# Optimization experiments

Measured on AMD Instinct MI355X. Metric: run time of the kernel, lower is better.

## Reference

```python
import jax, jax.numpy as jnp
import numpy as np
import math

N, D, H, DK, DV, FF = 2048, 1024, 16, 64, 64, 4096
EPS = 1e-5


def setup_inputs() -> dict:
    key = jax.random.key(0)
    ks = jax.random.split(key, 10)
    s = 0.02  # scaled init for numerical stability (original uses torch.randn)
    return {
        "x": jax.random.normal(ks[0], (N, D), dtype=jnp.float32),
        # per-head projections stacked: [H, D, DK/DV]
        "w_q": jax.random.normal(ks[1], (H, D, DK), dtype=jnp.float32) * s,
        "w_k": jax.random.normal(ks[2], (H, D, DK), dtype=jnp.float32) * s,
        "w_v": jax.random.normal(ks[3], (H, D, DV), dtype=jnp.float32) * s,
        "w_o": jax.random.normal(ks[4], (H * DV, D), dtype=jnp.float32) * s,
        "ln1_g": jnp.ones((D,), jnp.float32),
        "ln1_b": jnp.zeros((D,), jnp.float32),
        # FFN: Linear stored as [in, out] so y = x @ w + b
        "w1": jax.random.normal(ks[5], (D, FF), dtype=jnp.float32) * s,
        "b1": jnp.zeros((FF,), jnp.float32),
        "w2": jax.random.normal(ks[6], (FF, D), dtype=jnp.float32) * s,
        "b2": jnp.zeros((D,), jnp.float32),
        "ln2_g": jnp.ones((D,), jnp.float32),
        "ln2_b": jnp.zeros((D,), jnp.float32),
    }


def _layernorm(x, g, b):
    mu = jnp.mean(x, axis=-1, keepdims=True)
    var = jnp.mean(jnp.square(x - mu), axis=-1, keepdims=True)
    return (x - mu) * jax.lax.rsqrt(var + EPS) * g + b


def reference(x, w_q, w_k, w_v, w_o, ln1_g, ln1_b, w1, b1, w2, b2, ln2_g, ln2_b):
    n = x.shape[0]
    # multi-head causal self-attention (heads batched instead of Python loop)
    q = jnp.einsum('nd,hdk->hnk', x, w_q)  # [H,N,DK]
    k = jnp.einsum('nd,hdk->hnk', x, w_k)
    v = jnp.einsum('nd,hdv->hnv', x, w_v)
    scores = jnp.einsum('hnk,hmk->hnm', q, k) / math.sqrt(DK)  # [H,N,N]
    causal = jnp.tril(jnp.ones((n, n), dtype=bool))
    scores = jnp.where(causal, scores, -jnp.inf)
    probs = jax.nn.softmax(scores, axis=-1)
    attn = jnp.einsum('hnm,hmv->hnv', probs, v)  # [H,N,DV]
    concat = jnp.transpose(attn, (1, 0, 2)).reshape(n, H * DV)  # head-order concat
    mha = concat @ w_o  # [N,D]
    # residual + LN, FFN (note: ReLU after BOTH linears, as in the source)
    h = _layernorm(x + mha, ln1_g, ln1_b)
    ff = jax.nn.relu(jax.nn.relu(h @ w1 + b1) @ w2 + b2)
    return _layernorm(h + ff, ln2_g, ln2_b)
```

## Files before the change

kernel.cpp:

```cpp
#include <hip/hip_runtime.h>
#include <math.h>


#define NTOK   2048
#define DMODEL 1024
#define NHEAD  16
#define DHEAD  64
#define DFF    4096
#define LNEPS  1e-5f

typedef unsigned int   u32;
typedef unsigned short u16;
typedef _Float16       f16;
typedef __attribute__((ext_vector_type(8))) short short8;
typedef __attribute__((ext_vector_type(4))) float f32x4;
typedef __attribute__((ext_vector_type(4))) _Float16 f16x4;

__device__ __forceinline__ u16 f2b(float f) {
    u32 b = __float_as_uint(f);
    b += 0x7FFFu + ((b >> 16) & 1u);
    return (u16)(b >> 16);
}
__device__ __forceinline__ float b2f(u16 v) {
    return __uint_as_float((u32)v << 16);
}

#define AS1(p) ((const __attribute__((address_space(1))) u32*)(p))
#define AS3(p) ((__attribute__((address_space(3))) u32*)(p))

template<int RELU, int BIAS, int RESID, int OUT_BF16, int SPLITK>
__global__ __launch_bounds__(256) void mfma_gemm(
    const u16* __restrict__ A, int lda,
    const u16* __restrict__ Bt, int ldbt,
    void* __restrict__ Cp, int ldc, int Kc,
    const float* __restrict__ bias,
    const float* __restrict__ resid, int ldr,
    size_t pstride)
{
    __shared__ u16 As[2][128 * 32];
    __shared__ u16 Bs[2][128 * 32];

    const int tid = threadIdx.x;
    const int l = tid & 63, w = tid >> 6;
    const int row0 = blockIdx.y * 128, col0 = blockIdx.x * 128;
    const int kbase = (SPLITK > 1) ? blockIdx.z * Kc : 0;

    f32x4 acc[4][4];
    #pragma unroll
    for (int m = 0; m < 4; ++m)
        #pragma unroll
        for (int n = 0; n < 4; ++n)
            acc[m][n] = (f32x4){0.f, 0.f, 0.f, 0.f};

    const int srow = w * 32 + (l >> 2);
    const int skk  = (l & 3) * 8;
    const u16* Ag = A  + (size_t)(row0 + srow) * lda  + kbase + skk;
    const u16* Bg = Bt + (size_t)(col0 + srow) * ldbt + kbase + skk;

    const int fr  = l & 15;
    const int fk  = (l >> 4) * 8;
    const int ar0 = (w >> 1) * 64;
    const int bc0 = (w & 1) * 64;

    auto STAGE = [&](int buf, int k0) {
        char* AsB = (char*)&As[buf][0] + w * 2048;
        char* BsB = (char*)&Bs[buf][0] + w * 2048;
        __builtin_amdgcn_global_load_lds(AS1(Ag + k0),                     AS3(AsB),        16, 0, 0);
        __builtin_amdgcn_global_load_lds(AS1(Ag + k0 + (size_t)16 * lda),  AS3(AsB + 1024), 16, 0, 0);
        __builtin_amdgcn_global_load_lds(AS1(Bg + k0),                     AS3(BsB),        16, 0, 0);
        __builtin_amdgcn_global_load_lds(AS1(Bg + k0 + (size_t)16 * ldbt), AS3(BsB + 1024), 16, 0, 0);
    };

    STAGE(0, 0);
    int cur = 0;
    for (int k0 = 0; k0 < Kc; k0 += 32) {
        __syncthreads();
        if (k0 + 32 < Kc) STAGE(cur ^ 1, k0 + 32);

        short8 af[4], bfr[4];
        #pragma unroll
        for (int m = 0; m < 4; ++m)
            af[m] = *reinterpret_cast<const short8*>(&As[cur][(ar0 + m * 16 + fr) * 32 + fk]);
        #pragma unroll
        for (int n = 0; n < 4; ++n)
            bfr[n] = *reinterpret_cast<const short8*>(&Bs[cur][(bc0 + n * 16 + fr) * 32 + fk]);
        #pragma unroll
        for (int m = 0; m < 4; ++m)
            #pragma unroll
            for (int n = 0; n < 4; ++n)
                acc[m][n] = __builtin_amdgcn_mfma_f32_16x16x32_bf16(af[m], bfr[n], acc[m][n], 0, 0, 0);
        cur ^= 1;
    }

    if (SPLITK > 1) {
        f16* Pp = (f16*)Cp + blockIdx.z * pstride;
        #pragma unroll
        for (int m = 0; m < 4; ++m)
            #pragma unroll
            for (int n = 0; n < 4; ++n)
                #pragma unroll
                for (int r = 0; r < 4; ++r) {
                    int row = row0 + ar0 + m * 16 + (l >> 4) * 4 + r;
                    int col = col0 + bc0 + n * 16 + (l & 15);
                    Pp[(size_t)row * ldc + col] = (f16)acc[m][n][r];
                }
        return;
    }

    #pragma unroll
    for (int m = 0; m < 4; ++m) {
        #pragma unroll
        for (int n = 0; n < 4; ++n) {
            #pragma unroll
            for (int r = 0; r < 4; ++r) {
                int row = row0 + ar0 + m * 16 + (l >> 4) * 4 + r;
                int col = col0 + bc0 + n * 16 + (l & 15);
                float val = acc[m][n][r];
                if (BIAS)  val += bias[col];
                if (RESID) val += resid[(size_t)row * ldr + col];
                if (RELU)  val = fmaxf(val, 0.0f);
                if (OUT_BF16) ((u16*)Cp)[(size_t)row * ldc + col] = f2b(val);
                else          ((float*)Cp)[(size_t)row * ldc + col] = val;
            }
        }
    }
}

__device__ __forceinline__ void transpose_tile32(
    const float* __restrict__ in, int ldin,
    u16* __restrict__ out, int ldout, int r0, int c0)
{
    __shared__ float tile[32][33];
    int tx = threadIdx.x & 31, ty = threadIdx.x >> 5;
    #pragma unroll
    for (int i = 0; i < 4; ++i) {
        int r = ty + i * 8;
        tile[r][tx] = in[(size_t)(r0 + r) * ldin + c0 + tx];
    }
    __syncthreads();
    #pragma unroll
    for (int i = 0; i < 4; ++i) {
        int rr = ty + i * 8;
        out[(size_t)(c0 + rr) * ldout + r0 + tx] = f2b(tile[tx][rr]);
    }
}

__global__ __launch_bounds__(256) void prep_all(
    const float* __restrict__ x,
    const float* __restrict__ wq, const float* __restrict__ wk, const float* __restrict__ wv,
    const float* __restrict__ wo, const float* __restrict__ w1, const float* __restrict__ w2,
    u16* __restrict__ xb, u16* __restrict__ wqkvT, u16* __restrict__ woT,
    u16* __restrict__ w1T, u16* __restrict__ w2T)
{
    int b = blockIdx.x;
    if (b < 1024) {
        int i = (b * 256 + threadIdx.x) * 8;
        float4 v0 = *reinterpret_cast<const float4*>(x + i);
        float4 v1 = *reinterpret_cast<const float4*>(x + i + 4);
        ushort4 o0, o1;
        o0.x = f2b(v0.x); o0.y = f2b(v0.y); o0.z = f2b(v0.z); o0.w = f2b(v0.w);
        o1.x = f2b(v1.x); o1.y = f2b(v1.y); o1.z = f2b(v1.z); o1.w = f2b(v1.w);
        *reinterpret_cast<ushort4*>(xb + i)     = o0;
        *reinterpret_cast<ushort4*>(xb + i + 4) = o1;
    } else if (b < 4096) {
        int u = b - 1024;
        int z = u >> 6, t = u & 63;
        int p = z >> 4, hh = z & 15;
        const float* in = (p == 0 ? wq : p == 1 ? wk : wv) + (size_t)hh * DMODEL * DHEAD;
        u16* out = wqkvT + (size_t)(p * 1024 + hh * 64) * DMODEL;
        transpose_tile32(in, DHEAD, out, DMODEL, (t >> 1) * 32, (t & 1) * 32);
    } else if (b < 5120) {
        int u = b - 4096;
        transpose_tile32(wo, DMODEL, woT, DMODEL, (u >> 5) * 32, (u & 31) * 32);
    } else if (b < 9216) {
        int u = b - 5120;
        transpose_tile32(w1, DFF, w1T, DMODEL, (u >> 7) * 32, (u & 127) * 32);
    } else {
        int u = b - 9216;
        transpose_tile32(w2, DMODEL, w2T, DFF, (u >> 5) * 32, (u & 31) * 32);
    }
}

__global__ __launch_bounds__(512) void flash_attn_mfma(
    const u16* __restrict__ qkvb, u16* __restrict__ concatb)
{
    const int bid = blockIdx.x;
    const int lo = bid & 255;
    int it = lo >> 3;
    int h  = lo & 7;
    if (bid >= 256) { it = 31 - it; h += 8; }

    const u16* qh = qkvb + h * DHEAD;
    const u16* kh = qkvb + DMODEL + h * DHEAD;
    const u16* vh = qkvb + 2 * DMODEL + h * DHEAD;
    const int LDQ = 3 * DMODEL;

    const float SC2  = 0.18033688f;
    const float THR2 = 11.541560f;

    __shared__ u16 Ks[4][64][72];
    __shared__ u16 Vt[4][64][72];

    const int tid = threadIdx.x;
    const int l = tid & 63, w = tid >> 6;
    const int grp = w >> 2, wq = w & 3;
    const int fr = l & 15, fg = l >> 4;

    short8 qf[2];
    {
        const u16* qp = qh + (size_t)(it * 64 + wq * 16 + fr) * LDQ + fg * 8;
        qf[0] = *reinterpret_cast<const short8*>(qp);
        qf[1] = *reinterpret_cast<const short8*>(qp + 32);
    }

    const int kr  = tid >> 1;
    const int kb  = kr >> 6, krl = kr & 63;
    const int kc  = (tid & 1) * 32;
    const int vp  = tid >> 2;
    const int vb  = vp >> 5, vpl = vp & 31;
    const int vc  = (tid & 3) * 16;

    short8 kf[4], vf0[2], vf1[2];
    auto PREFETCH = [&](int s) {
        const u16* kg = kh + (size_t)(s * 256 + kr) * LDQ + kc;
        kf[0] = *reinterpret_cast<const short8*>(kg);
        kf[1] = *reinterpret_cast<const short8*>(kg + 8);
        kf[2] = *reinterpret_cast<const short8*>(kg + 16);
        kf[3] = *reinterpret_cast<const short8*>(kg + 24);
        const u16* vg = vh + (size_t)(s * 256 + 2 * vp) * LDQ + vc;
        vf0[0] = *reinterpret_cast<const short8*>(vg);
        vf0[1] = *reinterpret_cast<const short8*>(vg + 8);
        vf1[0] = *reinterpret_cast<const short8*>(vg + LDQ);
        vf1[1] = *reinterpret_cast<const short8*>(vg + LDQ + 8);
    };

    f32x4 o[4];
    #pragma unroll
    for (int n = 0; n < 4; ++n) o[n] = (f32x4){0.f, 0.f, 0.f, 0.f};
    float m_run = -INFINITY, l_run = 0.0f;

    const int sA = fr + 16 * ((2 * fg) & 3);
    const int sB = sA + 16;
    const bool hi = (fg >= 2);

    char* VtSb = (char*)&Vt[vb][0][0];

    const int niter = (it >> 2) + 1;
    PREFETCH(0);

    for (int s = 0; s < niter; ++s) {
        __syncthreads();
        *reinterpret_cast<short8*>(&Ks[kb][krl][kc +  0]) = kf[0];
        *reinterpret_cast<short8*>(&Ks[kb][krl][kc +  8]) = kf[1];
        *reinterpret_cast<short8*>(&Ks[kb][krl][kc + 16]) = kf[2];
        *reinterpret_cast<short8*>(&Ks[kb][krl][kc + 24]) = kf[3];
        #pragma unroll
        for (int c2 = 0; c2 < 2; ++c2) {
            #pragma unroll
            for (int i = 0; i < 8; ++i) {
                u32 word = (u32)(u16)vf0[c2][i] | ((u32)(u16)vf1[c2][i] << 16);
                int dv = vc + c2 * 8 + i;
                int off = 144 * dv + 16 * ((vpl >> 2) ^ ((dv >> 3) & 7)) + 4 * (vpl & 3);
                *reinterpret_cast<u32*>(VtSb + off) = word;
            }
        }
        if (s + 1 < niter) PREFETCH(s + 1);
        __syncthreads();

        #pragma unroll
        for (int t = 0; t < 2; ++t) {
            const int jt = 4 * s + 2 * grp + t;
            if (jt > it) continue;
            const int buf = 2 * grp + t;
            const u16 (*KsG)[72] = Ks[buf];
            char* VtG = (char*)&Vt[buf][0][0];

            f32x4 s_[4];
            #pragma unroll
            for (int n = 0; n < 4; ++n) s_[n] = (f32x4){0.f, 0.f, 0.f, 0.f};
            __builtin_amdgcn_s_setprio(1);
            #pragma unroll
            for (int n = 0; n < 4; ++n) {
                #pragma unroll
                for (int ks = 0; ks < 2; ++ks) {
                    short8 kfrag = *reinterpret_cast<const short8*>(&KsG[n * 16 + fr][ks * 32 + fg * 8]);
                    s_[n] = __builtin_amdgcn_mfma_f32_16x16x32_bf16(kfrag, qf[ks], s_[n], 0, 0, 0);
                }
            }
            __builtin_amdgcn_s_setprio(0);

            const bool diag = (jt == it);
            const int qrow_t = wq * 16 + fr;
            float sv[4][4];
            float pm = -INFINITY;
            #pragma unroll
            for (int n = 0; n < 4; ++n)
                #pragma unroll
                for (int r = 0; r < 4; ++r) {
                    float v = s_[n][r] * SC2;
                    if (diag && (n * 16 + fg * 4 + r) > qrow_t) v = -INFINITY;
                    sv[n][r] = v;
                    pm = fmaxf(pm, v);
                }
            pm = fmaxf(pm, __shfl_xor(pm, 16));
            pm = fmaxf(pm, __shfl_xor(pm, 32));
            if (!__all(pm <= m_run + THR2)) {
                float mnew = fmaxf(m_run, pm);
                float corr = exp2f(m_run - mnew);
                l_run *= corr;
                #pragma unroll
                for (int n = 0; n < 4; ++n) {
                    o[n][0] *= corr; o[n][1] *= corr; o[n][2] *= corr; o[n][3] *= corr;
                }
                m_run = mnew;
            }
            float rs = 0.0f;
            float pp[4][4];
            #pragma unroll
            for (int n = 0; n < 4; ++n)
                #pragma unroll
                for (int r = 0; r < 4; ++r) {
                    float pv = exp2f(sv[n][r] - m_run);
                    pp[n][r] = pv;
                    rs += pv;
                }
            rs += __shfl_xor(rs, 16);
            rs += __shfl_xor(rs, 32);
            l_run += rs;

            u32 pk[4][2];
            #pragma unroll
            for (int n = 0; n < 4; ++n) {
                pk[n][0] = (__float_as_uint(pp[n][0]) >> 16) | (__float_as_uint(pp[n][1]) & 0xFFFF0000u);
                pk[n][1] = (__float_as_uint(pp[n][2]) >> 16) | (__float_as_uint(pp[n][3]) & 0xFFFF0000u);
            }

            __builtin_amdgcn_s_setprio(1);
            #pragma unroll
            for (int ks = 0; ks < 2; ++ks) {
                u32 a0 = __shfl(pk[2 * ks][0], sA);
                u32 a1 = __shfl(pk[2 * ks][1], sA);
                u32 a2 = __shfl(pk[2 * ks][0], sB);
                u32 a3 = __shfl(pk[2 * ks][1], sB);
                u32 b0 = __shfl(pk[2 * ks + 1][0], sA);
                u32 b1 = __shfl(pk[2 * ks + 1][1], sA);
                u32 b2 = __shfl(pk[2 * ks + 1][0], sB);
                u32 b3 = __shfl(pk[2 * ks + 1][1], sB);
                union { u32 u[4]; short8 s8; } pb;
                pb.u[0] = hi ? b0 : a0;
                pb.u[1] = hi ? b1 : a1;
                pb.u[2] = hi ? b2 : a2;
                pb.u[3] = hi ? b3 : a3;
                #pragma unroll
                for (int n = 0; n < 4; ++n) {
                    int dv = n * 16 + fr;
                    const short8* vfrag = reinterpret_cast<const short8*>(
                        VtG + 144 * dv + 16 * ((ks * 4 + fg) ^ ((dv >> 3) & 7)));
                    o[n] = __builtin_amdgcn_mfma_f32_16x16x32_bf16(*vfrag, pb.s8, o[n], 0, 0, 0);
                }
            }
            __builtin_amdgcn_s_setprio(0);
        }
    }

    __syncthreads();
    float* mrg = reinterpret_cast<float*>(&Ks[0][0][0]);
    const int slot = (wq * 64 + l) * 18;
    if (grp == 1) {
        #pragma unroll
        for (int n = 0; n < 4; ++n)
            #pragma unroll
            for (int r = 0; r < 4; ++r)
                mrg[slot + n * 4 + r] = o[n][r];
        mrg[slot + 16] = m_run;
        mrg[slot + 17] = l_run;
    }
    __syncthreads();
    if (grp == 0) {
        float mB = mrg[slot + 16], lB = mrg[slot + 17];
        float mstar = fmaxf(m_run, mB);
        float cA = exp2f(m_run - mstar);
        float cB = exp2f(mB - mstar);
        float inv = 1.0f / (l_run * cA + lB * cB);
        int qrow = it * 64 + wq * 16 + fr;
        #pragma unroll
        for (int n = 0; n < 4; ++n)
            #pragma unroll
            for (int r = 0; r < 4; ++r) {
                float val = (o[n][r] * cA + mrg[slot + n * 4 + r] * cB) * inv;
                concatb[(size_t)qrow * DMODEL + h * DHEAD + n * 16 + fg * 4 + r] = f2b(val);
            }
    }
}

template<int NPART, int RELUB, int OUTF, int DUAL, int BASEBF16>
__global__ __launch_bounds__(256) void ln_fuse(
    const f16* __restrict__ P, size_t pstride,
    const void* __restrict__ basev,
    const float* __restrict__ bias2,
    const float* __restrict__ g, const float* __restrict__ b,
    float* __restrict__ out, u16* __restrict__ outb)
{
    int row = blockIdx.x, tid = threadIdx.x;
    __shared__ float red[256];
    size_t off = (size_t)row * DMODEL + tid * 4;

    float a0 = 0.f, a1 = 0.f, a2 = 0.f, a3 = 0.f;
    #pragma unroll
    for (int p = 0; p < NPART; ++p) {
        f16x4 t = *reinterpret_cast<const f16x4*>(P + (size_t)p * pstride + off);
        a0 += (float)t.x; a1 += (float)t.y; a2 += (float)t.z; a3 += (float)t.w;
    }
    if (RELUB) {
        float4 bb = *reinterpret_cast<const float4*>(bias2 + tid * 4);
        a0 = fmaxf(a0 + bb.x, 0.0f); a1 = fmaxf(a1 + bb.y, 0.0f);
        a2 = fmaxf(a2 + bb.z, 0.0f); a3 = fmaxf(a3 + bb.w, 0.0f);
    }
    float vals[4];
    if (BASEBF16) {
        ushort4 bs = *reinterpret_cast<const ushort4*>((const u16*)basev + off);
        vals[0] = a0 + b2f(bs.x); vals[1] = a1 + b2f(bs.y);
        vals[2] = a2 + b2f(bs.z); vals[3] = a3 + b2f(bs.w);
    } else {
        float4 bs = *reinterpret_cast<const float4*>((const float*)basev + off);
        vals[0] = a0 + bs.x; vals[1] = a1 + bs.y; vals[2] = a2 + bs.z; vals[3] = a3 + bs.w;
    }

    float s = vals[0] + vals[1] + vals[2] + vals[3];
    red[tid] = s; __syncthreads();
    for (int st = 128; st > 0; st >>= 1) { if (tid < st) red[tid] += red[tid + st]; __syncthreads(); }
    float mu = red[0] * (1.0f / DMODEL);
    __syncthreads();

    float vs = 0.0f;
    #pragma unroll
    for (int i = 0; i < 4; ++i) { float d = vals[i] - mu; vs += d * d; }
    red[tid] = vs; __syncthreads();
    for (int st = 128; st > 0; st >>= 1) { if (tid < st) red[tid] += red[tid + st]; __syncthreads(); }
    float rstd = rsqrtf(red[0] * (1.0f / DMODEL) + LNEPS);

    float4 gv = *reinterpret_cast<const float4*>(g + tid * 4);
    float4 bv = *reinterpret_cast<const float4*>(b + tid * 4);
    float gs[4] = {gv.x, gv.y, gv.z, gv.w};
    float bsc[4] = {bv.x, bv.y, bv.z, bv.w};
    #pragma unroll
    for (int i = 0; i < 4; ++i) {
        float r = (vals[i] - mu) * rstd * gs[i] + bsc[i];
        if (OUTF) out[off + i] = r;
        if (DUAL) outb[off + i] = f2b(r);
    }
}

extern "C" void kernel_launch(void* const* d_in, const int* in_sizes, int n_in,
                              void* d_out, int out_size, void* d_ws, size_t ws_size,
                              hipStream_t stream)
{
    const float* x    = (const float*)d_in[0];
    const float* wq   = (const float*)d_in[1];
    const float* wk   = (const float*)d_in[2];
    const float* wv   = (const float*)d_in[3];
    const float* wo   = (const float*)d_in[4];
    const float* ln1g = (const float*)d_in[5];
    const float* ln1b = (const float*)d_in[6];
    const float* w1   = (const float*)d_in[7];
    const float* b1   = (const float*)d_in[8];
    const float* w2   = (const float*)d_in[9];
    const float* b2   = (const float*)d_in[10];
    const float* ln2g = (const float*)d_in[11];
    const float* ln2b = (const float*)d_in[12];
    float* out = (float*)d_out;

    char* ws = (char*)d_ws;
    const size_t MB = 1024 * 1024;
    u16* w2T     = (u16*)(ws + 0 * MB);
    u16* w1T     = (u16*)(ws + 8 * MB);
    u16* woT     = (u16*)(ws + 16 * MB);
    u16* wqkvT   = (u16*)(ws + 18 * MB);
    u16* xb      = (u16*)(ws + 24 * MB);
    u16* ff1b    = (u16*)(ws + 24 * MB);
    u16* qkvb    = (u16*)(ws + 28 * MB);
    u16* concatb = (u16*)(ws + 40 * MB);
    f16* Ph      = (f16*)(ws + 44 * MB);
    f16* Fh      = (f16*)(ws + 44 * MB);
    u16* h1b     = (u16*)(ws + 60 * MB);

    const size_t PSTRIDE = (size_t)NTOK * DMODEL;

    dim3 blk(256);

    prep_all<<<dim3(13312), blk, 0, stream>>>(x, wq, wk, wv, wo, w1, w2,
                                              xb, wqkvT, woT, w1T, w2T);

    mfma_gemm<0,0,0,1,1><<<dim3(24, 16), blk, 0, stream>>>(
        xb, DMODEL, wqkvT, DMODEL, qkvb, 3 * DMODEL, DMODEL, nullptr, nullptr, 0, 0);
    flash_attn_mfma<<<dim3(512), dim3(512), 0, stream>>>(qkvb, concatb);
    mfma_gemm<0,0,0,0,4><<<dim3(8, 16, 4), blk, 0, stream>>>(
        concatb, DMODEL, woT, DMODEL, Ph, DMODEL, 256, nullptr, nullptr, 0, PSTRIDE);
    ln_fuse<4,0,0,1,0><<<dim3(NTOK), blk, 0, stream>>>(
        Ph, PSTRIDE, x, nullptr, ln1g, ln1b, nullptr, h1b);
    mfma_gemm<1,1,0,1,1><<<dim3(32, 16), blk, 0, stream>>>(
        h1b, DMODEL, w1T, DMODEL, ff1b, DFF, DMODEL, b1, nullptr, 0, 0);
    mfma_gemm<0,0,0,0,4><<<dim3(8, 16, 4), blk, 0, stream>>>(
        ff1b, DFF, w2T, DFF, Fh, DMODEL, 1024, nullptr, nullptr, 0, PSTRIDE);
    ln_fuse<4,1,1,0,1><<<dim3(NTOK), blk, 0, stream>>>(
        Fh, PSTRIDE, h1b, b2, ln2g, ln2b, out, nullptr);
}
```

Measured before the change: 162.3 us.

## Split flash-attention KV tiles across four wave groups with 1024-thread blocks

```diff
diff --git a/kernel.cpp b/kernel.cpp
--- a/kernel.cpp
+++ b/kernel.cpp
@@ -181,7 +181,7 @@
     }
 }
 
-__global__ __launch_bounds__(512) void flash_attn_mfma(
+__global__ __launch_bounds__(1024, 8) void flash_attn_mfma(
     const u16* __restrict__ qkvb, u16* __restrict__ concatb)
 {
     const int bid = blockIdx.x;
@@ -213,25 +213,21 @@
         qf[1] = *reinterpret_cast<const short8*>(qp + 32);
     }
 
-    const int kr  = tid >> 1;
+    const int kr  = tid >> 2;
     const int kb  = kr >> 6, krl = kr & 63;
-    const int kc  = (tid & 1) * 32;
-    const int vp  = tid >> 2;
+    const int kc  = (tid & 3) * 16;
+    const int vp  = tid >> 3;
     const int vb  = vp >> 5, vpl = vp & 31;
-    const int vc  = (tid & 3) * 16;
-
-    short8 kf[4], vf0[2], vf1[2];
+    const int vc  = (tid & 7) * 8;
+
+    short8 kf0, kf1, vf0, vf1;
     auto PREFETCH = [&](int s) {
         const u16* kg = kh + (size_t)(s * 256 + kr) * LDQ + kc;
-        kf[0] = *reinterpret_cast<const short8*>(kg);
-        kf[1] = *reinterpret_cast<const short8*>(kg + 8);
-        kf[2] = *reinterpret_cast<const short8*>(kg + 16);
-        kf[3] = *reinterpret_cast<const short8*>(kg + 24);
+        kf0 = *reinterpret_cast<const short8*>(kg);
+        kf1 = *reinterpret_cast<const short8*>(kg + 8);
         const u16* vg = vh + (size_t)(s * 256 + 2 * vp) * LDQ + vc;
-        vf0[0] = *reinterpret_cast<const short8*>(vg);
-        vf0[1] = *reinterpret_cast<const short8*>(vg + 8);
-        vf1[0] = *reinterpret_cast<const short8*>(vg + LDQ);
-        vf1[1] = *reinterpret_cast<const short8*>(vg + LDQ + 8);
+        vf0 = *reinterpret_cast<const short8*>(vg);
+        vf1 = *reinterpret_cast<const short8*>(vg + LDQ);
     };
 
     f32x4 o[4];
@@ -250,123 +246,115 @@
 
     for (int s = 0; s < niter; ++s) {
         __syncthreads();
-        *reinterpret_cast<short8*>(&Ks[kb][krl][kc +  0]) = kf[0];
-        *reinterpret_cast<short8*>(&Ks[kb][krl][kc +  8]) = kf[1];
-        *reinterpret_cast<short8*>(&Ks[kb][krl][kc + 16]) = kf[2];
-        *reinterpret_cast<short8*>(&Ks[kb][krl][kc + 24]) = kf[3];
-        #pragma unroll
-        for (int c2 = 0; c2 < 2; ++c2) {
-            #pragma unroll
-            for (int i = 0; i < 8; ++i) {
-                u32 word = (u32)(u16)vf0[c2][i] | ((u32)(u16)vf1[c2][i] << 16);
-                int dv = vc + c2 * 8 + i;
-                int off = 144 * dv + 16 * ((vpl >> 2) ^ ((dv >> 3) & 7)) + 4 * (vpl & 3);
-                *reinterpret_cast<u32*>(VtSb + off) = word;
-            }
+        *reinterpret_cast<short8*>(&Ks[kb][krl][kc])     = kf0;
+        *reinterpret_cast<short8*>(&Ks[kb][krl][kc + 8]) = kf1;
+        #pragma unroll
+        for (int i = 0; i < 8; ++i) {
+            u32 word = (u32)(u16)vf0[i] | ((u32)(u16)vf1[i] << 16);
+            int dv = vc + i;
+            int off = 144 * dv + 16 * ((vpl >> 2) ^ ((dv >> 3) & 7)) + 4 * (vpl & 3);
+            *reinterpret_cast<u32*>(VtSb + off) = word;
         }
         if (s + 1 < niter) PREFETCH(s + 1);
         __syncthreads();
 
-        #pragma unroll
-        for (int t = 0; t < 2; ++t) {
-            const int jt = 4 * s + 2 * grp + t;
-            if (jt > it) continue;
-            const int buf = 2 * grp + t;
-            const u16 (*KsG)[72] = Ks[buf];
-            char* VtG = (char*)&Vt[buf][0][0];
-
-            f32x4 s_[4];
-            #pragma unroll
-            for (int n = 0; n < 4; ++n) s_[n] = (f32x4){0.f, 0.f, 0.f, 0.f};
-            __builtin_amdgcn_s_setprio(1);
+        const int jt = 4 * s + grp;
+        if (jt > it) continue;
+        const u16 (*KsG)[72] = Ks[grp];
+        char* VtG = (char*)&Vt[grp][0][0];
+
+        f32x4 s_[4];
+        #pragma unroll
+        for (int n = 0; n < 4; ++n) s_[n] = (f32x4){0.f, 0.f, 0.f, 0.f};
+        __builtin_amdgcn_s_setprio(1);
+        #pragma unroll
+        for (int n = 0; n < 4; ++n) {
+            #pragma unroll
+            for (int ks = 0; ks < 2; ++ks) {
+                short8 kfrag = *reinterpret_cast<const short8*>(&KsG[n * 16 + fr][ks * 32 + fg * 8]);
+                s_[n] = __builtin_amdgcn_mfma_f32_16x16x32_bf16(kfrag, qf[ks], s_[n], 0, 0, 0);
+            }
+        }
+        __builtin_amdgcn_s_setprio(0);
+
+        const bool diag = (jt == it);
+        const int qrow_t = wq * 16 + fr;
+        float sv[4][4];
+        float pm = -INFINITY;
+        #pragma unroll
+        for (int n = 0; n < 4; ++n)
+            #pragma unroll
+            for (int r = 0; r < 4; ++r) {
+                float v = s_[n][r] * SC2;
+                if (diag && (n * 16 + fg * 4 + r) > qrow_t) v = -INFINITY;
+                sv[n][r] = v;
+                pm = fmaxf(pm, v);
+            }
+        pm = fmaxf(pm, __shfl_xor(pm, 16));
+        pm = fmaxf(pm, __shfl_xor(pm, 32));
+        if (!__all(pm <= m_run + THR2)) {
+            float mnew = fmaxf(m_run, pm);
+            float corr = exp2f(m_run - mnew);
+            l_run *= corr;
             #pragma unroll
             for (int n = 0; n < 4; ++n) {
-                #pragma unroll
-                for (int ks = 0; ks < 2; ++ks) {
-                    short8 kfrag = *reinterpret_cast<const short8*>(&KsG[n * 16 + fr][ks * 32 + fg * 8]);
-                    s_[n] = __builtin_amdgcn_mfma_f32_16x16x32_bf16(kfrag, qf[ks], s_[n], 0, 0, 0);
-                }
+                o[n][0] *= corr; o[n][1] *= corr; o[n][2] *= corr; o[n][3] *= corr;
             }
-            __builtin_amdgcn_s_setprio(0);
-
-            const bool diag = (jt == it);
-            const int qrow_t = wq * 16 + fr;
-            float sv[4][4];
-            float pm = -INFINITY;
-            #pragma unroll
-            for (int n = 0; n < 4; ++n)
-                #pragma unroll
-                for (int r = 0; r < 4; ++r) {
-                    float v = s_[n][r] * SC2;
-                    if (diag && (n * 16 + fg * 4 + r) > qrow_t) v = -INFINITY;
-                    sv[n][r] = v;
-                    pm = fmaxf(pm, v);
-                }
-            pm = fmaxf(pm, __shfl_xor(pm, 16));
-            pm = fmaxf(pm, __shfl_xor(pm, 32));
-            if (!__all(pm <= m_run + THR2)) {
-                float mnew = fmaxf(m_run, pm);
-                float corr = exp2f(m_run - mnew);
-                l_run *= corr;
-                #pragma unroll
-                for (int n = 0; n < 4; ++n) {
-                    o[n][0] *= corr; o[n][1] *= corr; o[n][2] *= corr; o[n][3] *= corr;
-                }
-                m_run = mnew;
+            m_run = mnew;
+        }
+        float rs = 0.0f;
+        float pp[4][4];
+        #pragma unroll
+        for (int n = 0; n < 4; ++n)
+            #pragma unroll
+            for (int r = 0; r < 4; ++r) {
+                float pv = exp2f(sv[n][r] - m_run);
+                pp[n][r] = pv;
+                rs += pv;
             }
-            float rs = 0.0f;
-            float pp[4][4];
-            #pragma unroll
-            for (int n = 0; n < 4; ++n)
-                #pragma unroll
-                for (int r = 0; r < 4; ++r) {
-                    float pv = exp2f(sv[n][r] - m_run);
-                    pp[n][r] = pv;
-                    rs += pv;
-                }
-            rs += __shfl_xor(rs, 16);
-            rs += __shfl_xor(rs, 32);
-            l_run += rs;
-
-            u32 pk[4][2];
+        rs += __shfl_xor(rs, 16);
+        rs += __shfl_xor(rs, 32);
+        l_run += rs;
+
+        u32 pk[4][2];
+        #pragma unroll
+        for (int n = 0; n < 4; ++n) {
+            pk[n][0] = (__float_as_uint(pp[n][0]) >> 16) | (__float_as_uint(pp[n][1]) & 0xFFFF0000u);
+            pk[n][1] = (__float_as_uint(pp[n][2]) >> 16) | (__float_as_uint(pp[n][3]) & 0xFFFF0000u);
+        }
+
+        __builtin_amdgcn_s_setprio(1);
+        #pragma unroll
+        for (int ks = 0; ks < 2; ++ks) {
+            u32 a0 = __shfl(pk[2 * ks][0], sA);
+            u32 a1 = __shfl(pk[2 * ks][1], sA);
+            u32 a2 = __shfl(pk[2 * ks][0], sB);
+            u32 a3 = __shfl(pk[2 * ks][1], sB);
+            u32 b0 = __shfl(pk[2 * ks + 1][0], sA);
+            u32 b1 = __shfl(pk[2 * ks + 1][1], sA);
+            u32 b2 = __shfl(pk[2 * ks + 1][0], sB);
+            u32 b3 = __shfl(pk[2 * ks + 1][1], sB);
+            union { u32 u[4]; short8 s8; } pb;
+            pb.u[0] = hi ? b0 : a0;
+            pb.u[1] = hi ? b1 : a1;
+            pb.u[2] = hi ? b2 : a2;
+            pb.u[3] = hi ? b3 : a3;
             #pragma unroll
             for (int n = 0; n < 4; ++n) {
-                pk[n][0] = (__float_as_uint(pp[n][0]) >> 16) | (__float_as_uint(pp[n][1]) & 0xFFFF0000u);
-                pk[n][1] = (__float_as_uint(pp[n][2]) >> 16) | (__float_as_uint(pp[n][3]) & 0xFFFF0000u);
+                int dv = n * 16 + fr;
+                const short8* vfrag = reinterpret_cast<const short8*>(
+                    VtG + 144 * dv + 16 * ((ks * 4 + fg) ^ ((dv >> 3) & 7)));
+                o[n] = __builtin_amdgcn_mfma_f32_16x16x32_bf16(*vfrag, pb.s8, o[n], 0, 0, 0);
             }
-
-            __builtin_amdgcn_s_setprio(1);
-            #pragma unroll
-            for (int ks = 0; ks < 2; ++ks) {
-                u32 a0 = __shfl(pk[2 * ks][0], sA);
-                u32 a1 = __shfl(pk[2 * ks][1], sA);
-                u32 a2 = __shfl(pk[2 * ks][0], sB);
-                u32 a3 = __shfl(pk[2 * ks][1], sB);
-                u32 b0 = __shfl(pk[2 * ks + 1][0], sA);
-                u32 b1 = __shfl(pk[2 * ks + 1][1], sA);
-                u32 b2 = __shfl(pk[2 * ks + 1][0], sB);
-                u32 b3 = __shfl(pk[2 * ks + 1][1], sB);
-                union { u32 u[4]; short8 s8; } pb;
-                pb.u[0] = hi ? b0 : a0;
-                pb.u[1] = hi ? b1 : a1;
-                pb.u[2] = hi ? b2 : a2;
-                pb.u[3] = hi ? b3 : a3;
-                #pragma unroll
-                for (int n = 0; n < 4; ++n) {
-                    int dv = n * 16 + fr;
-                    const short8* vfrag = reinterpret_cast<const short8*>(
-                        VtG + 144 * dv + 16 * ((ks * 4 + fg) ^ ((dv >> 3) & 7)));
-                    o[n] = __builtin_amdgcn_mfma_f32_16x16x32_bf16(*vfrag, pb.s8, o[n], 0, 0, 0);
-                }
-            }
-            __builtin_amdgcn_s_setprio(0);
-        }
-    }
-
-    __syncthreads();
+        }
+        __builtin_amdgcn_s_setprio(0);
+    }
+
     float* mrg = reinterpret_cast<float*>(&Ks[0][0][0]);
-    const int slot = (wq * 64 + l) * 18;
-    if (grp == 1) {
+    const int slotL = (wq * 64 + l) * 18;
+    const int slotH = (256 + wq * 64 + l) * 18;
+
+    auto WRITE = [&](int slot) {
         #pragma unroll
         for (int n = 0; n < 4; ++n)
             #pragma unroll
@@ -374,22 +362,42 @@
                 mrg[slot + n * 4 + r] = o[n][r];
         mrg[slot + 16] = m_run;
         mrg[slot + 17] = l_run;
-    }
+    };
+    auto MERGE = [&](int slot) {
+        float m2 = mrg[slot + 16];
+        if (m2 > -INFINITY) {
+            float l2 = mrg[slot + 17];
+            float mstar = fmaxf(m_run, m2);
+            float cA = exp2f(m_run - mstar);
+            float cB = exp2f(m2 - mstar);
+            #pragma unroll
+            for (int n = 0; n < 4; ++n)
+                #pragma unroll
+                for (int r = 0; r < 4; ++r)
+                    o[n][r] = o[n][r] * cA + mrg[slot + n * 4 + r] * cB;
+            l_run = l_run * cA + l2 * cB;
+            m_run = mstar;
+        }
+    };
+
+    __syncthreads();
+    if (grp == 1) WRITE(slotL);
+    if (grp == 3) WRITE(slotH);
+    __syncthreads();
+    if (grp == 0) MERGE(slotL);
+    if (grp == 2) MERGE(slotH);
+    __syncthreads();
+    if (grp == 2) WRITE(slotL);
     __syncthreads();
     if (grp == 0) {
-        float mB = mrg[slot + 16], lB = mrg[slot + 17];
-        float mstar = fmaxf(m_run, mB);
-        float cA = exp2f(m_run - mstar);
-        float cB = exp2f(mB - mstar);
-        float inv = 1.0f / (l_run * cA + lB * cB);
+        MERGE(slotL);
+        float inv = 1.0f / l_run;
         int qrow = it * 64 + wq * 16 + fr;
         #pragma unroll
         for (int n = 0; n < 4; ++n)
             #pragma unroll
-            for (int r = 0; r < 4; ++r) {
-                float val = (o[n][r] * cA + mrg[slot + n * 4 + r] * cB) * inv;
-                concatb[(size_t)qrow * DMODEL + h * DHEAD + n * 16 + fg * 4 + r] = f2b(val);
-            }
+            for (int r = 0; r < 4; ++r)
+                concatb[(size_t)qrow * DMODEL + h * DHEAD + n * 16 + fg * 4 + r] = f2b(o[n][r] * inv);
     }
 }
 
@@ -493,7 +501,7 @@
 
     mfma_gemm<0,0,0,1,1><<<dim3(24, 16), blk, 0, stream>>>(
         xb, DMODEL, wqkvT, DMODEL, qkvb, 3 * DMODEL, DMODEL, nullptr, nullptr, 0, 0);
-    flash_attn_mfma<<<dim3(512), dim3(512), 0, stream>>>(qkvb, concatb);
+    flash_attn_mfma<<<dim3(512), dim3(1024), 0, stream>>>(qkvb, concatb);
     mfma_gemm<0,0,0,0,4><<<dim3(8, 16, 4), blk, 0, stream>>>(
         concatb, DMODEL, woT, DMODEL, Ph, DMODEL, 256, nullptr, nullptr, 0, PSTRIDE);
     ln_fuse<4,0,0,1,0><<<dim3(NTOK), blk, 0, stream>>>(
```

After: 210.5 us. 1.3x slower.
